# Performance work log

Measured on AMD Instinct MI355X. Metric: run time of the kernel, lower is better.

## Reference

```python
import jax, jax.numpy as jnp
import numpy as np

N_NODES = 500_000
N_FEAT = 125          # embedding dim; cat with pos(3) -> 128
HIDDEN = 128
OUT_DIM = 64
N_TYPES = 100
N_GRAPHS = 4096


def setup_inputs() -> dict:
    key = jax.random.key(0)
    ks = jax.random.split(key, 10)
    pos = jax.random.normal(ks[0], (N_NODES, 3), dtype=jnp.float32)
    z = jax.random.randint(ks[1], (N_NODES,), 0, N_TYPES)
    batch = jnp.sort(jax.random.randint(ks[2], (N_NODES,), 0, N_GRAPHS))
    emb = jax.random.normal(ks[3], (N_TYPES, N_FEAT), dtype=jnp.float32)
    s1 = 1.0 / np.sqrt(N_FEAT + 3)
    s2 = 1.0 / np.sqrt(HIDDEN)
    W1 = jax.random.normal(ks[4], (N_FEAT + 3, HIDDEN), dtype=jnp.float32) * s1
    b1 = jnp.zeros((HIDDEN,), dtype=jnp.float32)
    W2 = jax.random.normal(ks[5], (HIDDEN, HIDDEN), dtype=jnp.float32) * s2
    b2 = jnp.zeros((HIDDEN,), dtype=jnp.float32)
    W3 = jax.random.normal(ks[6], (HIDDEN, OUT_DIM), dtype=jnp.float32) * s2
    b3 = jnp.zeros((OUT_DIM,), dtype=jnp.float32)
    return {"pos": pos, "z": z, "batch": batch, "emb": emb,
            "W1": W1, "b1": b1, "W2": W2, "b2": b2, "W3": W3, "b3": b3}


def reference(pos, z, batch, emb, W1, b1, W2, b2, W3, b3):
    # embed node types and concat with 3D positions  -> [N, 128]
    x = jnp.concatenate([pos, emb[z]], axis=-1)
    # two equivariant-transformer layers (per-node transform) + relu
    x = jax.nn.relu(x @ W1 + b1)   # [N, H]
    x = jax.nn.relu(x @ W2 + b2)   # [N, H]
    # output head
    x = x @ W3 + b3                # [N, O]
    # global mean pool per graph
    s = jax.ops.segment_sum(x, batch, num_segments=N_GRAPHS)                    # [G, O]
    cnt = jax.ops.segment_sum(jnp.ones((x.shape[0], 1), x.dtype), batch,
                              num_segments=N_GRAPHS)                            # [G, 1]
    return s / jnp.maximum(cnt, 1.0)
```

## Files before the change

kernel.cpp:

```cpp
#include <hip/hip_runtime.h>
#include <hip/hip_bf16.h>

#define N_NODES 500000
#define N_FEAT 125
#define HID 128
#define OUTD 64
#define N_GRAPHS 4096
#define N_TYPES 100
#define WTILE 32
#define NTILES32 (N_NODES / WTILE)
#define NBLOCKS 256
#define NWAVES 8
#define WPAD 136

typedef float f32x4 __attribute__((ext_vector_type(4)));
typedef short s16x8 __attribute__((ext_vector_type(8)));

#define OFF_T 0
#define SZ_T (N_TYPES * WPAD * 2)
#define OFF_W2 (OFF_T + SZ_T)
#define OFF_W3 (OFF_W2 + HID * WPAD * 2)
#define OFF_B2 (OFF_W3 + OUTD * WPAD * 2)
#define OFF_SCR (OFF_B2 + HID * 4)
#define SCR_BYTES (WTILE * WPAD * 2)
#define LDS_BYTES (OFF_SCR + NWAVES * SCR_BYTES)

#define WS_GSUM 0
#define WS_GCNT ((size_t)N_GRAPHS * OUTD * 4)
#define WS_T    (WS_GCNT + (size_t)N_GRAPHS * 4)
#define WS_ZERO WS_T

__device__ __forceinline__ unsigned short f2bf(float f) {
  union { float f; unsigned u; } v; v.f = f;
  unsigned r = v.u + 0x7FFFu + ((v.u >> 16) & 1u);
  return (unsigned short)(r >> 16);
}
__device__ __forceinline__ float bf2f(unsigned short u) {
  union { unsigned u; float f; } v; v.u = ((unsigned)u) << 16;
  return v.f;
}
__device__ __forceinline__ unsigned pk2bf(float a, float b) {
  __hip_bfloat162 h = __float22bfloat162_rn(float2{a, b});
  union { __hip_bfloat162 h; unsigned u; } v; v.h = h;
  return v.u;
}

__device__ __forceinline__ void wavefence() {
  __builtin_amdgcn_sched_barrier(0);
  __builtin_amdgcn_wave_barrier();
  __builtin_amdgcn_sched_barrier(0);
}

extern "C" __global__ void gnn_prep(const float* __restrict__ emb,
                                    const float* __restrict__ W1,
                                    const float* __restrict__ b1,
                                    unsigned short* __restrict__ Tg)
{
  const int g = blockIdx.x, j = threadIdx.x;
  float acc = b1[j];
  const float* er = emb + g * N_FEAT;
  for (int k = 0; k < N_FEAT; ++k)
    acc = fmaf(er[k], W1[(3 + k) * HID + j], acc);
  Tg[g * HID + j] = f2bf(acc);
}

extern "C" __global__ void __launch_bounds__(512, 2)
gnn_main(const float* __restrict__ pos, const int* __restrict__ z,
         const int* __restrict__ batch, const unsigned short* __restrict__ Tg,
         const float* __restrict__ W1, const float* __restrict__ W2,
         const float* __restrict__ b2, const float* __restrict__ W3,
         float* __restrict__ gsum, int* __restrict__ gcnt)
{
  extern __shared__ char lds[];
  unsigned short* Tl  = (unsigned short*)(lds + OFF_T);
  unsigned short* w2t = (unsigned short*)(lds + OFF_W2);
  unsigned short* w3t = (unsigned short*)(lds + OFF_W3);
  float* bias2 = (float*)(lds + OFF_B2);

  const int t = threadIdx.x;

  for (int i = t; i < N_TYPES * HID; i += 512) {
    int g = i >> 7, f = i & 127;
    Tl[g * WPAD + f] = Tg[i];
  }
  for (int i = t; i < HID * HID; i += 512) {
    int k = i >> 7, n = i & 127;
    w2t[n * WPAD + k] = f2bf(W2[i]);
  }
  for (int i = t; i < HID * OUTD; i += 512) {
    int k = i >> 6, n = i & 63;
    w3t[n * WPAD + k] = f2bf(W3[i]);
  }
  if (t < HID) bias2[t] = b2[t];

  const int wave = t >> 6, lane = t & 63, quad = lane >> 4, l15 = lane & 15;
  unsigned short* xs = (unsigned short*)(lds + OFF_SCR + wave * SCR_BYTES);

  float w1r[3][4][8];
  #pragma unroll
  for (int c = 0; c < 3; ++c)
    #pragma unroll
    for (int k = 0; k < 4; ++k)
      #pragma unroll
      for (int j = 0; j < 8; ++j)
        w1r[c][k][j] = W1[c * HID + k * 32 + quad * 8 + j];

  __syncthreads();

  const int gwave = blockIdx.x * NWAVES + wave;

  for (int tile = gwave; tile < NTILES32; tile += NBLOCKS * NWAVES) {
    const int base = tile * WTILE;

    const int id0 = batch[base + l15];
    const int id1 = batch[base + 16 + l15];

    s16x8 a[2][4];
    #pragma unroll
    for (int m = 0; m < 2; ++m) {
      const int node = base + m * 16 + l15;
      const int zi = z[node];
      const float px = pos[node * 3], py = pos[node * 3 + 1], pz = pos[node * 3 + 2];
      const unsigned short* Tr = Tl + zi * WPAD;
      #pragma unroll
      for (int k = 0; k < 4; ++k) {
        s16x8 tf = *(const s16x8*)(Tr + k * 32 + quad * 8);
        s16x8 fr;
        #pragma unroll
        for (int j = 0; j < 8; j += 2) {
          float v0 = bf2f((unsigned short)tf[j])
                   + px * w1r[0][k][j] + py * w1r[1][k][j] + pz * w1r[2][k][j];
          float v1 = bf2f((unsigned short)tf[j + 1])
                   + px * w1r[0][k][j + 1] + py * w1r[1][k][j + 1] + pz * w1r[2][k][j + 1];
          ((unsigned*)&fr)[j >> 1] = pk2bf(fmaxf(v0, 0.f), fmaxf(v1, 0.f));
        }
        a[m][k] = fr;
      }
    }

    f32x4 acc[8][2] = {};
    __builtin_amdgcn_s_setprio(1);
    #pragma unroll
    for (int oi = 0; oi < 8; ++oi)
      #pragma unroll
      for (int k = 0; k < 4; ++k) {
        s16x8 w = *(const s16x8*)(w2t + (oi * 16 + l15) * WPAD + k * 32 + quad * 8);
        acc[oi][0] = __builtin_amdgcn_mfma_f32_16x16x32_bf16(w, a[0][k], acc[oi][0], 0, 0, 0);
        acc[oi][1] = __builtin_amdgcn_mfma_f32_16x16x32_bf16(w, a[1][k], acc[oi][1], 0, 0, 0);
      }
    __builtin_amdgcn_s_setprio(0);
    #pragma unroll
    for (int oi = 0; oi < 8; ++oi) {
      const int f0 = oi * 16 + quad * 4;
      f32x4 bv = *(const f32x4*)(bias2 + f0);
      #pragma unroll
      for (int m = 0; m < 2; ++m) {
        unsigned lo = pk2bf(fmaxf(acc[oi][m][0] + bv[0], 0.f),
                            fmaxf(acc[oi][m][1] + bv[1], 0.f));
        unsigned hi = pk2bf(fmaxf(acc[oi][m][2] + bv[2], 0.f),
                            fmaxf(acc[oi][m][3] + bv[3], 0.f));
        *(uint2*)(xs + (m * 16 + l15) * WPAD + f0) = uint2{lo, hi};
      }
    }
    wavefence();
    #pragma unroll
    for (int m = 0; m < 2; ++m)
      #pragma unroll
      for (int k = 0; k < 4; ++k)
        a[m][k] = *(const s16x8*)(xs + (m * 16 + l15) * WPAD + k * 32 + quad * 8);
    wavefence();

    f32x4 acc3[4][2] = {};
    __builtin_amdgcn_s_setprio(1);
    #pragma unroll
    for (int oi = 0; oi < 4; ++oi)
      #pragma unroll
      for (int k = 0; k < 4; ++k) {
        s16x8 w = *(const s16x8*)(w3t + (oi * 16 + l15) * WPAD + k * 32 + quad * 8);
        acc3[oi][0] = __builtin_amdgcn_mfma_f32_16x16x32_bf16(w, a[0][k], acc3[oi][0], 0, 0, 0);
        acc3[oi][1] = __builtin_amdgcn_mfma_f32_16x16x32_bf16(w, a[1][k], acc3[oi][1], 0, 0, 0);
      }
    __builtin_amdgcn_s_setprio(0);

    {
      int done = 0;
      while (done < 32) {
        const int g = __builtin_amdgcn_readfirstlane(batch[base + done]);
        const bool m0 = (id0 == g), m1 = (id1 == g);
        float red[4][4];
        #pragma unroll
        for (int oi = 0; oi < 4; ++oi)
          #pragma unroll
          for (int r = 0; r < 4; ++r)
            red[oi][r] = (m0 ? acc3[oi][0][r] : 0.f) + (m1 ? acc3[oi][1][r] : 0.f);
        #pragma unroll
        for (int s = 1; s <= 8; s <<= 1)
          #pragma unroll
          for (int oi = 0; oi < 4; ++oi)
            #pragma unroll
            for (int r = 0; r < 4; ++r)
              red[oi][r] += __shfl_xor(red[oi][r], s, 64);
        const int cnt = (int)((__popcll(__ballot(m0)) + __popcll(__ballot(m1))) >> 2);
        if (l15 == 0) {
          #pragma unroll
          for (int oi = 0; oi < 4; ++oi)
            #pragma unroll
            for (int r = 0; r < 4; ++r)
              atomicAdd(&gsum[g * OUTD + oi * 16 + quad * 4 + r], red[oi][r]);
        }
        if (lane == 0) atomicAdd(&gcnt[g], cnt);
        done += cnt;
      }
    }
  }
}

extern "C" __global__ void gnn_finalize(const float* __restrict__ gsum,
                                        const int* __restrict__ gcnt,
                                        const float* __restrict__ b3,
                                        float* __restrict__ out)
{
  int i = blockIdx.x * 256 + threadIdx.x;
  if (i < N_GRAPHS * OUTD) {
    int g = i >> 6, o = i & 63;
    int c = gcnt[g];
    out[i] = (c > 0) ? (gsum[i] / (float)c + b3[o]) : 0.f;
  }
}

extern "C" void kernel_launch(void* const* d_in, const int* in_sizes, int n_in,
                              void* d_out, int out_size, void* d_ws, size_t ws_size,
                              hipStream_t stream) {
  const float* pos  = (const float*)d_in[0];
  const int*   z    = (const int*)d_in[1];
  const int*   batch= (const int*)d_in[2];
  const float* emb  = (const float*)d_in[3];
  const float* W1   = (const float*)d_in[4];
  const float* b1   = (const float*)d_in[5];
  const float* W2   = (const float*)d_in[6];
  const float* b2   = (const float*)d_in[7];
  const float* W3   = (const float*)d_in[8];
  const float* b3   = (const float*)d_in[9];

  float* gsum = (float*)d_ws;
  int*   gcnt = (int*)((char*)d_ws + WS_GCNT);
  unsigned short* Tg = (unsigned short*)((char*)d_ws + WS_T);

  hipMemsetAsync(d_ws, 0, WS_ZERO, stream);

  hipLaunchKernelGGL(gnn_prep, dim3(N_TYPES), dim3(HID), 0, stream, emb, W1, b1, Tg);

  hipFuncSetAttribute((const void*)gnn_main,
                      hipFuncAttributeMaxDynamicSharedMemorySize, LDS_BYTES);
  hipLaunchKernelGGL(gnn_main, dim3(NBLOCKS), dim3(512), LDS_BYTES, stream,
                     pos, z, batch, Tg, W1, W2, b2, W3, gsum, gcnt);
  hipLaunchKernelGGL(gnn_finalize, dim3((N_GRAPHS * OUTD + 255) / 256), dim3(256), 0, stream,
                     gsum, gcnt, b3, (float*)d_out);
}
```

Baseline: 147.7 us.

## Feed layer-2 MFMA output directly into layer-3 MFMA, drop LDS round trip

Layer-2 results are now kept in registers as packed bf16 fragments and fed straight into 16x16x16 bf16 MFMAs for layer 3. This removes the per-wave LDS scratch write/read and its wave barriers, using a W3 layout pre-swizzled to match the accumulator fragment layout. It also folds the workspace memset into the prep kernel to save a launch, and reads segment ids via readlane instead of reloading batch from memory. The cost is twice as many smaller MFMAs for layer 3, plus extra register pressure from holding the packed fragments.

New measurement: 137.4 us. 1.07x faster.

```diff
diff --git a/kernel.cpp b/kernel.cpp
--- a/kernel.cpp
+++ b/kernel.cpp
@@ -15,20 +15,20 @@
 
 typedef float f32x4 __attribute__((ext_vector_type(4)));
 typedef short s16x8 __attribute__((ext_vector_type(8)));
+typedef short s16x4 __attribute__((ext_vector_type(4)));
 
 #define OFF_T 0
 #define SZ_T (N_TYPES * WPAD * 2)
 #define OFF_W2 (OFF_T + SZ_T)
-#define OFF_W3 (OFF_W2 + HID * WPAD * 2)
-#define OFF_B2 (OFF_W3 + OUTD * WPAD * 2)
-#define OFF_SCR (OFF_B2 + HID * 4)
-#define SCR_BYTES (WTILE * WPAD * 2)
-#define LDS_BYTES (OFF_SCR + NWAVES * SCR_BYTES)
+#define OFF_W3K (OFF_W2 + HID * WPAD * 2)
+#define OFF_B2 (OFF_W3K + 4 * 8 * 64 * 8)
+#define LDS_BYTES (OFF_B2 + HID * 4)
 
 #define WS_GSUM 0
 #define WS_GCNT ((size_t)N_GRAPHS * OUTD * 4)
 #define WS_T    (WS_GCNT + (size_t)N_GRAPHS * 4)
 #define WS_ZERO WS_T
+#define WS_ZERO_V4 (WS_ZERO / 16)
 
 __device__ __forceinline__ unsigned short f2bf(float f) {
   union { float f; unsigned u; } v; v.f = f;
@@ -44,24 +44,28 @@
   union { __hip_bfloat162 h; unsigned u; } v; v.h = h;
   return v.u;
 }
-
-__device__ __forceinline__ void wavefence() {
-  __builtin_amdgcn_sched_barrier(0);
-  __builtin_amdgcn_wave_barrier();
-  __builtin_amdgcn_sched_barrier(0);
+__device__ __forceinline__ s16x4 u2frag(uint2 v) {
+  union { uint2 u; s16x4 s; } c; c.u = v; return c.s;
 }
 
 extern "C" __global__ void gnn_prep(const float* __restrict__ emb,
                                     const float* __restrict__ W1,
                                     const float* __restrict__ b1,
-                                    unsigned short* __restrict__ Tg)
+                                    unsigned short* __restrict__ Tg,
+                                    f32x4* __restrict__ wsz)
 {
-  const int g = blockIdx.x, j = threadIdx.x;
-  float acc = b1[j];
-  const float* er = emb + g * N_FEAT;
-  for (int k = 0; k < N_FEAT; ++k)
-    acc = fmaf(er[k], W1[(3 + k) * HID + j], acc);
-  Tg[g * HID + j] = f2bf(acc);
+  const int j = threadIdx.x;
+  const int tid = blockIdx.x * 128 + j;
+  for (int i = tid; i < WS_ZERO_V4; i += 256 * 128)
+    wsz[i] = (f32x4){0.f, 0.f, 0.f, 0.f};
+  const int g = blockIdx.x;
+  if (g < N_TYPES) {
+    float acc = b1[j];
+    const float* er = emb + g * N_FEAT;
+    for (int k = 0; k < N_FEAT; ++k)
+      acc = fmaf(er[k], W1[(3 + k) * HID + j], acc);
+    Tg[g * HID + j] = f2bf(acc);
+  }
 }
 
 extern "C" __global__ void __launch_bounds__(512, 2)
@@ -74,7 +78,7 @@
   extern __shared__ char lds[];
   unsigned short* Tl  = (unsigned short*)(lds + OFF_T);
   unsigned short* w2t = (unsigned short*)(lds + OFF_W2);
-  unsigned short* w3t = (unsigned short*)(lds + OFF_W3);
+  uint2* w3k = (uint2*)(lds + OFF_W3K);
   float* bias2 = (float*)(lds + OFF_B2);
 
   const int t = threadIdx.x;
@@ -87,14 +91,19 @@
     int k = i >> 7, n = i & 127;
     w2t[n * WPAD + k] = f2bf(W2[i]);
   }
-  for (int i = t; i < HID * OUTD; i += 512) {
-    int k = i >> 6, n = i & 63;
-    w3t[n * WPAD + k] = f2bf(W3[i]);
+  for (int i = t; i < 4 * 8 * 64; i += 512) {
+    int ob = i >> 9, rest = i & 511;
+    int oi = rest >> 6, ln = rest & 63;
+    int q = ln >> 4, l = ln & 15;
+    int f0 = oi * 16 + q * 4, o = ob * 16 + l;
+    uint2 v;
+    v.x = pk2bf(W3[(f0 + 0) * OUTD + o], W3[(f0 + 1) * OUTD + o]);
+    v.y = pk2bf(W3[(f0 + 2) * OUTD + o], W3[(f0 + 3) * OUTD + o]);
+    w3k[i] = v;
   }
   if (t < HID) bias2[t] = b2[t];
 
   const int wave = t >> 6, lane = t & 63, quad = lane >> 4, l15 = lane & 15;
-  unsigned short* xs = (unsigned short*)(lds + OFF_SCR + wave * SCR_BYTES);
 
   float w1r[3][4][8];
   #pragma unroll
@@ -138,75 +147,66 @@
       }
     }
 
-    f32x4 acc[8][2] = {};
+    uint2 pb[8][2];
     __builtin_amdgcn_s_setprio(1);
     #pragma unroll
-    for (int oi = 0; oi < 8; ++oi)
+    for (int oi = 0; oi < 8; ++oi) {
+      f32x4 c0 = {}, c1 = {};
       #pragma unroll
       for (int k = 0; k < 4; ++k) {
         s16x8 w = *(const s16x8*)(w2t + (oi * 16 + l15) * WPAD + k * 32 + quad * 8);
-        acc[oi][0] = __builtin_amdgcn_mfma_f32_16x16x32_bf16(w, a[0][k], acc[oi][0], 0, 0, 0);
-        acc[oi][1] = __builtin_amdgcn_mfma_f32_16x16x32_bf16(w, a[1][k], acc[oi][1], 0, 0, 0);
-      }
-    __builtin_amdgcn_s_setprio(0);
-    #pragma unroll
-    for (int oi = 0; oi < 8; ++oi) {
+        c0 = __builtin_amdgcn_mfma_f32_16x16x32_bf16(w, a[0][k], c0, 0, 0, 0);
+        c1 = __builtin_amdgcn_mfma_f32_16x16x32_bf16(w, a[1][k], c1, 0, 0, 0);
+      }
       const int f0 = oi * 16 + quad * 4;
       f32x4 bv = *(const f32x4*)(bias2 + f0);
-      #pragma unroll
-      for (int m = 0; m < 2; ++m) {
-        unsigned lo = pk2bf(fmaxf(acc[oi][m][0] + bv[0], 0.f),
-                            fmaxf(acc[oi][m][1] + bv[1], 0.f));
-        unsigned hi = pk2bf(fmaxf(acc[oi][m][2] + bv[2], 0.f),
-                            fmaxf(acc[oi][m][3] + bv[3], 0.f));
-        *(uint2*)(xs + (m * 16 + l15) * WPAD + f0) = uint2{lo, hi};
-      }
+      pb[oi][0].x = pk2bf(fmaxf(c0[0] + bv[0], 0.f), fmaxf(c0[1] + bv[1], 0.f));
+      pb[oi][0].y = pk2bf(fmaxf(c0[2] + bv[2], 0.f), fmaxf(c0[3] + bv[3], 0.f));
+      pb[oi][1].x = pk2bf(fmaxf(c1[0] + bv[0], 0.f), fmaxf(c1[1] + bv[1], 0.f));
+      pb[oi][1].y = pk2bf(fmaxf(c1[2] + bv[2], 0.f), fmaxf(c1[3] + bv[3], 0.f));
     }
-    wavefence();
-    #pragma unroll
-    for (int m = 0; m < 2; ++m)
-      #pragma unroll
-      for (int k = 0; k < 4; ++k)
-        a[m][k] = *(const s16x8*)(xs + (m * 16 + l15) * WPAD + k * 32 + quad * 8);
-    wavefence();
+    __builtin_amdgcn_s_setprio(0);
 
     f32x4 acc3[4][2] = {};
     __builtin_amdgcn_s_setprio(1);
     #pragma unroll
-    for (int oi = 0; oi < 4; ++oi)
-      #pragma unroll
-      for (int k = 0; k < 4; ++k) {
-        s16x8 w = *(const s16x8*)(w3t + (oi * 16 + l15) * WPAD + k * 32 + quad * 8);
-        acc3[oi][0] = __builtin_amdgcn_mfma_f32_16x16x32_bf16(w, a[0][k], acc3[oi][0], 0, 0, 0);
-        acc3[oi][1] = __builtin_amdgcn_mfma_f32_16x16x32_bf16(w, a[1][k], acc3[oi][1], 0, 0, 0);
+    for (int ob = 0; ob < 4; ++ob)
+      #pragma unroll
+      for (int oi = 0; oi < 8; ++oi) {
+        s16x4 wa = u2frag(w3k[(ob * 8 + oi) * 64 + lane]);
+        acc3[ob][0] = __builtin_amdgcn_mfma_f32_16x16x16bf16_1k(
+            wa, u2frag(pb[oi][0]), acc3[ob][0], 0, 0, 0);
+        acc3[ob][1] = __builtin_amdgcn_mfma_f32_16x16x16bf16_1k(
+            wa, u2frag(pb[oi][1]), acc3[ob][1], 0, 0, 0);
       }
     __builtin_amdgcn_s_setprio(0);
 
     {
       int done = 0;
-      while (done < 32) {
-        const int g = __builtin_amdgcn_readfirstlane(batch[base + done]);
+      while (done < WTILE) {
+        const int srcv = (done < 16) ? id0 : id1;
+        const int g = __builtin_amdgcn_readlane(srcv, done & 15);
         const bool m0 = (id0 == g), m1 = (id1 == g);
         float red[4][4];
         #pragma unroll
-        for (int oi = 0; oi < 4; ++oi)
+        for (int ob = 0; ob < 4; ++ob)
           #pragma unroll
           for (int r = 0; r < 4; ++r)
-            red[oi][r] = (m0 ? acc3[oi][0][r] : 0.f) + (m1 ? acc3[oi][1][r] : 0.f);
+            red[ob][r] = (m0 ? acc3[ob][0][r] : 0.f) + (m1 ? acc3[ob][1][r] : 0.f);
         #pragma unroll
         for (int s = 1; s <= 8; s <<= 1)
           #pragma unroll
-          for (int oi = 0; oi < 4; ++oi)
+          for (int ob = 0; ob < 4; ++ob)
             #pragma unroll
             for (int r = 0; r < 4; ++r)
-              red[oi][r] += __shfl_xor(red[oi][r], s, 64);
+              red[ob][r] += __shfl_xor(red[ob][r], s, 64);
         const int cnt = (int)((__popcll(__ballot(m0)) + __popcll(__ballot(m1))) >> 2);
         if (l15 == 0) {
           #pragma unroll
-          for (int oi = 0; oi < 4; ++oi)
+          for (int ob = 0; ob < 4; ++ob)
             #pragma unroll
             for (int r = 0; r < 4; ++r)
-              atomicAdd(&gsum[g * OUTD + oi * 16 + quad * 4 + r], red[oi][r]);
+              atomicAdd(&gsum[g * OUTD + ob * 16 + quad * 4 + r], red[ob][r]);
         }
         if (lane == 0) atomicAdd(&gcnt[g], cnt);
         done += cnt;
@@ -246,9 +246,8 @@
   int*   gcnt = (int*)((char*)d_ws + WS_GCNT);
   unsigned short* Tg = (unsigned short*)((char*)d_ws + WS_T);
 
-  hipMemsetAsync(d_ws, 0, WS_ZERO, stream);
-
-  hipLaunchKernelGGL(gnn_prep, dim3(N_TYPES), dim3(HID), 0, stream, emb, W1, b1, Tg);
+  hipLaunchKernelGGL(gnn_prep, dim3(256), dim3(HID), 0, stream,
+                     emb, W1, b1, Tg, (f32x4*)d_ws);
 
   hipFuncSetAttribute((const void*)gnn_main,
                       hipFuncAttributeMaxDynamicSharedMemorySize, LDS_BYTES);
```
